# Performance work log

Hardware: AMD Instinct MI355X
Metric: run time of the kernel (lower is better)

The kernel has to match this reference:

```python
import jax, jax.numpy as jnp
from jax import lax
import numpy as np

D_MODEL = 768
D_STATE = 64
D_CONV = 4
EXPAND = 2
HEADDIM = 128
NGROUPS = 1
D_INNER = EXPAND * D_MODEL            # 1536
NHEADS = D_INNER // HEADDIM           # 12
D_IN_PROJ = 2 * D_INNER + 2 * NGROUPS * D_STATE + NHEADS  # 3212
CONV_DIM = D_INNER + 2 * NGROUPS * D_STATE                # 1664
BATCH, SEQLEN = 2, 4096
EPS = 1e-5


def setup_inputs() -> dict:
    key = jax.random.key(0)
    ks = jax.random.split(key, 8)
    u = jax.random.normal(ks[0], (BATCH, SEQLEN, D_MODEL), jnp.float32)
    W_in = jax.random.normal(ks[1], (D_IN_PROJ, D_MODEL), jnp.float32) * 0.02
    conv_w = jax.random.normal(ks[2], (CONV_DIM, D_CONV), jnp.float32) * 0.2
    conv_b = jnp.zeros((CONV_DIM,), jnp.float32)
    # dt_bias init as in BaseMambaBlock: inv-softplus of dt ~ logU(dt_min, dt_max)
    dt = jnp.exp(jax.random.uniform(ks[3], (NHEADS,)) * (np.log(0.1) - np.log(0.001)) + np.log(0.001))
    dt = jnp.clip(dt, 1e-4, None)
    dt_bias = dt + jnp.log(-jnp.expm1(-dt))
    A_log = jnp.log(jnp.abs(jax.random.normal(ks[4], (NHEADS,), jnp.float32)))
    Dp = jnp.ones((NHEADS,), jnp.float32)
    norm_w = jnp.ones((D_INNER,), jnp.float32)
    W_out = jax.random.normal(ks[5], (D_MODEL, D_INNER), jnp.float32) * 0.02
    return dict(u=u, W_in=W_in, conv_w=conv_w, conv_b=conv_b, dt_bias=dt_bias,
                A_log=A_log, Dp=Dp, norm_w=norm_w, W_out=W_out)


def _silu(x):
    return x * jax.nn.sigmoid(x)


def _depthwise_causal_conv(x, w, b):
    # x: [B, L, C], w: [C, W], b: [C]. Causal: left-pad W-1, crop to L.
    Bt, L, C = x.shape
    xp = jnp.pad(x, ((0, 0), (D_CONV - 1, 0), (0, 0)))
    # stack D_CONV shifted views: [B, L, C, W]
    taps = jnp.stack([xp[:, k:k + L, :] for k in range(D_CONV)], axis=-1)
    return jnp.einsum('blcw,cw->blc', taps, w) + b


def reference(u, W_in, conv_w, conv_b, dt_bias, A_log, Dp, norm_w, W_out):
    Bt, L, _ = u.shape
    zxbcdt = jnp.einsum('bld,ed->ble', u, W_in)  # [B, L, 3212]
    z = zxbcdt[..., :D_INNER]                                   # [B,L,1536]
    xBC = zxbcdt[..., D_INNER:D_INNER + CONV_DIM]               # [B,L,1664]
    dt = zxbcdt[..., D_INNER + CONV_DIM:]                       # [B,L,H]
    dt = jax.nn.softplus(dt + dt_bias)                          # [B,L,H]

    xBC = _silu(_depthwise_causal_conv(xBC, conv_w, conv_b))
    x = xBC[..., :D_INNER].reshape(Bt, L, NHEADS, HEADDIM)      # [B,L,H,P]
    Bm = xBC[..., D_INNER:D_INNER + NGROUPS * D_STATE]          # [B,L,N] (ngroups=1)
    Cm = xBC[..., D_INNER + NGROUPS * D_STATE:]                 # [B,L,N]

    A = -jnp.exp(A_log)                                         # [H]
    dA = jnp.exp(dt * A)                                        # [B,L,H]

    # time-major scan over the selective-state-space recurrence
    xs = (jnp.swapaxes(x, 0, 1),   # [L,B,H,P]
          jnp.swapaxes(dt, 0, 1),  # [L,B,H]
          jnp.swapaxes(dA, 0, 1),  # [L,B,H]
          jnp.swapaxes(Bm, 0, 1),  # [L,B,N]
          jnp.swapaxes(Cm, 0, 1))  # [L,B,N]

    def step(state, inp):
        x_t, dt_t, dA_t, B_t, C_t = inp
        # state: [B,H,P,N]
        state = state * dA_t[..., None, None] + (dt_t[..., None] * x_t)[..., None] * B_t[:, None, None, :]
        y_t = jnp.einsum('bhpn,bn->bhp', state, C_t)
        return state, y_t

    state0 = jnp.zeros((Bt, NHEADS, HEADDIM, D_STATE), u.dtype)
    _, y = lax.scan(step, state0, xs)                           # y: [L,B,H,P]
    y = jnp.swapaxes(y, 0, 1) + Dp[None, None, :, None] * x     # skip term D*x
    y = y.reshape(Bt, L, D_INNER)

    # RMSNormGated, norm_before_gate=False: normalize(y * silu(z)) * weight
    g = y * _silu(z)
    g = g * jax.lax.rsqrt(jnp.mean(g * g, axis=-1, keepdims=True) + EPS) * norm_w
    return jnp.einsum('bli,di->bld', g, W_out)
```

## Files before the change

kernel.cpp:

```cpp
#include <hip/hip_runtime.h>
#include <hip/hip_bf16.h>
#include <stdint.h>

#define BATCH   2
#define SEQLEN  4096
#define DMODEL  768
#define DSTATE  64
#define DCONV   4
#define HEADDIM 128
#define NHEADS  12
#define DINNER  1536
#define DINPROJ 3212
#define CONVDIM 1664
#define DXBC    1676
#define NPAD1   3328
#define ROWS    (BATCH*SEQLEN)
#define CHUNK   64
#define NCHUNK  (SEQLEN/CHUNK)
#define CROWS   8

typedef __bf16 bf16x8 __attribute__((ext_vector_type(8)));
typedef float  f32x4  __attribute__((ext_vector_type(4)));

__device__ __forceinline__ f32x4 splat4(float v) { return (f32x4){v, v, v, v}; }

__device__ __forceinline__ void load_lds16(const void* g, void* l) {
    __builtin_amdgcn_global_load_lds(
        (const __attribute__((address_space(1))) unsigned int*)g,
        (__attribute__((address_space(3))) unsigned int*)l, 16, 0, 0);
}

__global__ void cvt_bf16_kernel(const float* __restrict__ src,
                                __hip_bfloat16* __restrict__ dst, int n) {
    int i = (blockIdx.x * blockDim.x + threadIdx.x) * 4;
    if (i + 3 < n) {
        float4 v = *(const float4*)(src + i);
        dst[i + 0] = __float2bfloat16(v.x);
        dst[i + 1] = __float2bfloat16(v.y);
        dst[i + 2] = __float2bfloat16(v.z);
        dst[i + 3] = __float2bfloat16(v.w);
    } else {
        for (; i < n; ++i) dst[i] = __float2bfloat16(src[i]);
    }
}

__global__ void padw1_kernel(const float* __restrict__ src,
                             __hip_bfloat16* __restrict__ dst) {
    int i = blockIdx.x * blockDim.x + threadIdx.x;
    if (i >= NPAD1 * DMODEL) return;
    int r = i / DMODEL;
    float v = (r < DINPROJ) ? src[i] : 0.f;
    dst[i] = __float2bfloat16(v);
}

__global__ __launch_bounds__(256) void gemm_bf16_nt(
    const __hip_bfloat16* __restrict__ A,
    const __hip_bfloat16* __restrict__ Bt,
    float* __restrict__ C,
    int M, int Nreal, int K, int ldc)
{
    __shared__ __align__(16) __hip_bfloat16 As[128 * 32];
    __shared__ __align__(16) __hip_bfloat16 Bs[128 * 32];
    const int tid  = threadIdx.x;
    const int lane = tid & 63;
    const int wave = tid >> 6;
    const int wm   = wave >> 1;
    const int wn   = wave & 1;
    const int tm   = blockIdx.x * 128;
    const int tn   = blockIdx.y * 128;

    f32x4 acc[4][4] = {};

    const int lrow = tid >> 2;
    const int lk8  = (tid & 3) * 8;
    const __hip_bfloat16* gA0 = A  + (size_t)(tm + lrow)      * K + lk8;
    const __hip_bfloat16* gA1 = A  + (size_t)(tm + lrow + 64) * K + lk8;
    const __hip_bfloat16* gB0 = Bt + (size_t)(tn + lrow)      * K + lk8;
    const __hip_bfloat16* gB1 = Bt + (size_t)(tn + lrow + 64) * K + lk8;
    __hip_bfloat16* sA0 = As + tid * 8;
    __hip_bfloat16* sA1 = As + tid * 8 + 2048;
    __hip_bfloat16* sB0 = Bs + tid * 8;
    __hip_bfloat16* sB1 = Bs + tid * 8 + 2048;

    const int fr = lane & 15;
    const int fk = (lane >> 4) * 8;

    for (int kk = 0; kk < K; kk += 32) {
        load_lds16(gA0 + kk, sA0);
        load_lds16(gA1 + kk, sA1);
        load_lds16(gB0 + kk, sB0);
        load_lds16(gB1 + kk, sB1);
        __syncthreads();
        bf16x8 af[4], bfr[4];
#pragma unroll
        for (int i = 0; i < 4; ++i) {
            af[i]  = *(const bf16x8*)(As + (wm * 64 + i * 16 + fr) * 32 + fk);
            bfr[i] = *(const bf16x8*)(Bs + (wn * 64 + i * 16 + fr) * 32 + fk);
        }
#pragma unroll
        for (int mi = 0; mi < 4; ++mi)
#pragma unroll
            for (int ni = 0; ni < 4; ++ni)
                acc[mi][ni] = __builtin_amdgcn_mfma_f32_16x16x32_bf16(
                    af[mi], bfr[ni], acc[mi][ni], 0, 0, 0);
        __syncthreads();
    }

    const int rq = (lane >> 4) * 4;
#pragma unroll
    for (int mi = 0; mi < 4; ++mi) {
#pragma unroll
        for (int ni = 0; ni < 4; ++ni) {
            int col = tn + wn * 64 + ni * 16 + fr;
            if (col < Nreal) {
                size_t rbase = (size_t)(tm + wm * 64 + mi * 16 + rq) * ldc + col;
#pragma unroll
                for (int j = 0; j < 4; ++j)
                    C[rbase + (size_t)j * ldc] = acc[mi][ni][j];
            }
        }
    }
}

__global__ __launch_bounds__(256) void gemm1_fused(
    const __hip_bfloat16* __restrict__ A,
    const __hip_bfloat16* __restrict__ Bt,
    float* __restrict__ Cz,
    float* __restrict__ Cx)
{
    __shared__ __align__(16) __hip_bfloat16 As[128 * 32];
    __shared__ __align__(16) __hip_bfloat16 Bs[128 * 32];
    const int tid  = threadIdx.x;
    const int lane = tid & 63;
    const int wave = tid >> 6;
    const int wm   = wave >> 1;
    const int wn   = wave & 1;
    const int tm   = blockIdx.x * 128;
    const int tn   = blockIdx.y * 128;
    const int K    = DMODEL;

    float* Co;
    int ldc2, cb, nb;
    if (tn < DINNER) { Co = Cz; ldc2 = DINNER; cb = tn;          nb = DINNER; }
    else             { Co = Cx; ldc2 = DXBC;   cb = tn - DINNER; nb = DXBC;   }

    f32x4 acc[4][4] = {};

    const int lrow = tid >> 2;
    const int lk8  = (tid & 3) * 8;
    const __hip_bfloat16* gA0 = A  + (size_t)(tm + lrow)      * K + lk8;
    const __hip_bfloat16* gA1 = A  + (size_t)(tm + lrow + 64) * K + lk8;
    const __hip_bfloat16* gB0 = Bt + (size_t)(tn + lrow)      * K + lk8;
    const __hip_bfloat16* gB1 = Bt + (size_t)(tn + lrow + 64) * K + lk8;
    __hip_bfloat16* sA0 = As + tid * 8;
    __hip_bfloat16* sA1 = As + tid * 8 + 2048;
    __hip_bfloat16* sB0 = Bs + tid * 8;
    __hip_bfloat16* sB1 = Bs + tid * 8 + 2048;

    const int fr = lane & 15;
    const int fk = (lane >> 4) * 8;

    for (int kk = 0; kk < K; kk += 32) {
        load_lds16(gA0 + kk, sA0);
        load_lds16(gA1 + kk, sA1);
        load_lds16(gB0 + kk, sB0);
        load_lds16(gB1 + kk, sB1);
        __syncthreads();
        bf16x8 af[4], bfr[4];
#pragma unroll
        for (int i = 0; i < 4; ++i) {
            af[i]  = *(const bf16x8*)(As + (wm * 64 + i * 16 + fr) * 32 + fk);
            bfr[i] = *(const bf16x8*)(Bs + (wn * 64 + i * 16 + fr) * 32 + fk);
        }
#pragma unroll
        for (int mi = 0; mi < 4; ++mi)
#pragma unroll
            for (int ni = 0; ni < 4; ++ni)
                acc[mi][ni] = __builtin_amdgcn_mfma_f32_16x16x32_bf16(
                    af[mi], bfr[ni], acc[mi][ni], 0, 0, 0);
        __syncthreads();
    }

    const int rq = (lane >> 4) * 4;
#pragma unroll
    for (int mi = 0; mi < 4; ++mi) {
#pragma unroll
        for (int ni = 0; ni < 4; ++ni) {
            int col = cb + wn * 64 + ni * 16 + fr;
            if (col < nb) {
                size_t rbase = (size_t)(tm + wm * 64 + mi * 16 + rq) * ldc2 + col;
#pragma unroll
                for (int j = 0; j < 4; ++j)
                    Co[rbase + (size_t)j * ldc2] = acc[mi][ni][j];
            }
        }
    }
}

__global__ void conv_kernel(const float* __restrict__ xbcdt,
                            const float* __restrict__ convw,
                            const float* __restrict__ convb,
                            float* __restrict__ xbuf,
                            float* __restrict__ Bm,
                            float* __restrict__ Cm)
{
    int c = blockIdx.x * 256 + threadIdx.x;
    if (c >= CONVDIM) return;
    size_t row0 = (size_t)blockIdx.y * CROWS;
    int l0 = (int)(row0 & (SEQLEN - 1));
    float w0 = convw[c * 4 + 0];
    float w1 = convw[c * 4 + 1];
    float w2 = convw[c * 4 + 2];
    float w3 = convw[c * 4 + 3];
    float bias = convb[c];
    const float* src = xbcdt + row0 * DXBC + c;
    float x0 = (l0 >= 3) ? src[-3 * DXBC] : 0.f;
    float x1 = (l0 >= 2) ? src[-2 * DXBC] : 0.f;
    float x2 = (l0 >= 1) ? src[-1 * DXBC] : 0.f;
#pragma unroll
    for (int r = 0; r < CROWS; ++r) {
        float x3 = src[(size_t)r * DXBC];
        float acc = bias + x0 * w0 + x1 * w1 + x2 * w2 + x3 * w3;
        float v = acc / (1.f + __expf(-acc));
        size_t row = row0 + r;
        if (c < DINNER)               xbuf[row * DINNER + c] = v;
        else if (c < DINNER + DSTATE) Bm[row * DSTATE + (c - DINNER)] = v;
        else                          Cm[row * DSTATE + (c - DINNER - DSTATE)] = v;
        x0 = x1; x1 = x2; x2 = x3;
    }
}

__global__ void dt_kernel(const float* __restrict__ xbcdt,
                          const float* __restrict__ dt_bias,
                          const float* __restrict__ A_log,
                          float* __restrict__ dtb, float* __restrict__ dAb)
{
    int i = blockIdx.x * 256 + threadIdx.x;
    if (i >= ROWS * NHEADS) return;
    int row = i / NHEADS, h = i - row * NHEADS;
    float v = xbcdt[(size_t)row * DXBC + CONVDIM + h] + dt_bias[h];
    float dt = (v > 20.f) ? v : log1pf(__expf(v));
    float A = -__expf(A_log[h]);
    dtb[i] = dt;
    dAb[i] = __expf(dt * A);
}

__global__ __launch_bounds__(256) void chunk_state_f32(
    const float* __restrict__ xbuf, const float* __restrict__ Bm,
    const float* __restrict__ dtb, const float* __restrict__ dAb,
    float* __restrict__ Sloc, float* __restrict__ Pk)
{
    const int blk = blockIdx.x;
    const int k   = blk % NCHUNK;
    const int bh  = blk / NCHUNK;
    const int h   = bh % NHEADS;
    const int b   = bh / NHEADS;
    const int tid = threadIdx.x;
    const int pg  = tid >> 3;
    const int n0  = (tid & 7) * 8;
    const size_t row0 = (size_t)b * SEQLEN + k * CHUNK;
    const float* xbase = xbuf + (row0 * NHEADS + h) * HEADDIM + pg * 4;

    __shared__ __align__(16) float lB[CHUNK][DSTATE];
    __shared__ float lDA[CHUNK];
    __shared__ float ldt[CHUNK];

    for (int i = tid; i < CHUNK * DSTATE / 4; i += 256)
        ((float4*)&lB[0][0])[i] = ((const float4*)(Bm + row0 * DSTATE))[i];
    if (tid < CHUNK) {
        lDA[tid] = dAb[(row0 + tid) * NHEADS + h];
        ldt[tid] = dtb[(row0 + tid) * NHEADS + h];
    }
    __syncthreads();

    f32x4 s4[4][2] = {};
    f32x4 xt0[4], xt1[4];

#pragma unroll
    for (int tt = 0; tt < 4; ++tt)
        xt0[tt] = *(const f32x4*)(xbase + (size_t)tt * (NHEADS * HEADDIM));

#pragma unroll
    for (int tile = 0; tile < 16; ++tile) {
        f32x4* cur = (tile & 1) ? xt1 : xt0;
        f32x4* nxt = (tile & 1) ? xt0 : xt1;
        if (tile < 15) {
#pragma unroll
            for (int tt = 0; tt < 4; ++tt)
                nxt[tt] = *(const f32x4*)(xbase +
                    (size_t)((tile + 1) * 4 + tt) * (NHEADS * HEADDIM));
        }
#pragma unroll
        for (int tt = 0; tt < 4; ++tt) {
            int t = tile * 4 + tt;
            f32x4 da4 = splat4(lDA[t]);
            float dtv = ldt[t];
            f32x4 bv0 = *(const f32x4*)&lB[t][n0];
            f32x4 bv1 = *(const f32x4*)&lB[t][n0 + 4];
#pragma unroll
            for (int pl = 0; pl < 4; ++pl) {
                f32x4 dtx = splat4(dtv * cur[tt][pl]);
                s4[pl][0] = s4[pl][0] * da4 + dtx * bv0;
                s4[pl][1] = s4[pl][1] * da4 + dtx * bv1;
            }
        }
    }

    const size_t kbase = (size_t)(bh * NCHUNK + k) * (HEADDIM * DSTATE);
#pragma unroll
    for (int pl = 0; pl < 4; ++pl) {
        size_t a = kbase + (size_t)(pg * 4 + pl) * DSTATE + n0;
        *(f32x4*)(Sloc + a)     = s4[pl][0];
        *(f32x4*)(Sloc + a + 4) = s4[pl][1];
    }

    if (tid == 0) {
        float pr = 1.f;
#pragma unroll 8
        for (int t = 0; t < CHUNK; ++t) pr *= lDA[t];
        Pk[bh * NCHUNK + k] = pr;
    }
}

__global__ __launch_bounds__(256) void scan_phase2(
    float* __restrict__ Sloc, const float* __restrict__ Pk)
{
    int bh = blockIdx.x >> 5;
    int eo = (blockIdx.x & 31) * 256 + threadIdx.x;
    __shared__ float lP[NCHUNK];
    if (threadIdx.x < NCHUNK) lP[threadIdx.x] = Pk[bh * NCHUNK + threadIdx.x];
    __syncthreads();
    float s = 0.f;
    size_t base = (size_t)bh * NCHUNK * 8192 + eo;
#pragma unroll 8
    for (int k = 0; k < NCHUNK; ++k) {
        size_t a = base + (size_t)k * 8192;
        float f = Sloc[a];
        Sloc[a] = s;
        s = s * lP[k] + f;
    }
}

__global__ __launch_bounds__(256) void chunk_y_f32(
    const float* __restrict__ xbuf, const float* __restrict__ Bm,
    const float* __restrict__ Cm, const float* __restrict__ dtb,
    const float* __restrict__ dAb, const float* __restrict__ Dp,
    const float* __restrict__ Sini, float* __restrict__ ybuf)
{
    const int blk = blockIdx.x;
    const int kp  = blk % (NCHUNK / 2);
    const int bh  = blk / (NCHUNK / 2);
    const int h   = bh % NHEADS;
    const int b   = bh / NHEADS;
    const int tid = threadIdx.x;
    const int sub = tid >> 7;
    const int t2  = tid & 127;
    const int pg  = t2 >> 2;
    const int q   = t2 & 3;
    const int n0  = q * 16;
    const int ro  = sub * CHUNK;
    const size_t prow0 = (size_t)b * SEQLEN + (size_t)kp * 2 * CHUNK;
    const size_t row0  = prow0 + ro;
    const float* xbase = xbuf + (row0 * NHEADS + h) * HEADDIM + pg * 4;
    float* ybase = ybuf + (row0 * NHEADS + h) * HEADDIM + pg * 4;

    __shared__ __align__(16) float lB[2 * CHUNK][DSTATE];
    __shared__ __align__(16) float lC[2 * CHUNK][DSTATE];
    __shared__ float lDA[2 * CHUNK];
    __shared__ float ldt[2 * CHUNK];

    for (int i = tid; i < 2 * CHUNK * DSTATE / 4; i += 256) {
        ((float4*)&lB[0][0])[i] = ((const float4*)(Bm + prow0 * DSTATE))[i];
        ((float4*)&lC[0][0])[i] = ((const float4*)(Cm + prow0 * DSTATE))[i];
    }
    if (tid < 2 * CHUNK) {
        lDA[tid] = dAb[(prow0 + tid) * NHEADS + h];
        ldt[tid] = dtb[(prow0 + tid) * NHEADS + h];
    }

    f32x4 s4[4][4];
    const size_t kbase = (size_t)(bh * NCHUNK + kp * 2 + sub) * (HEADDIM * DSTATE);
#pragma unroll
    for (int pl = 0; pl < 4; ++pl) {
        size_t a = kbase + (size_t)(pg * 4 + pl) * DSTATE + n0;
#pragma unroll
        for (int nq = 0; nq < 4; ++nq)
            s4[pl][nq] = *(const f32x4*)(Sini + a + nq * 4);
    }
    const float dph = Dp[h];

    f32x4 xt0[4], xt1[4];
#pragma unroll
    for (int tt = 0; tt < 4; ++tt)
        xt0[tt] = *(const f32x4*)(xbase + (size_t)tt * (NHEADS * HEADDIM));
    __syncthreads();

#pragma unroll
    for (int tile = 0; tile < 16; ++tile) {
        f32x4* cur = (tile & 1) ? xt1 : xt0;
        f32x4* nxt = (tile & 1) ? xt0 : xt1;
        if (tile < 15) {
#pragma unroll
            for (int tt = 0; tt < 4; ++tt)
                nxt[tt] = *(const f32x4*)(xbase +
                    (size_t)((tile + 1) * 4 + tt) * (NHEADS * HEADDIM));
        }
#pragma unroll
        for (int tt = 0; tt < 4; ++tt) {
            int t = tile * 4 + tt;
            int tr = ro + t;
            f32x4 da4 = splat4(lDA[tr]);
            float dtv = ldt[tr];
            f32x4 bv0 = *(const f32x4*)&lB[tr][n0];
            f32x4 bv1 = *(const f32x4*)&lB[tr][n0 + 4];
            f32x4 bv2 = *(const f32x4*)&lB[tr][n0 + 8];
            f32x4 bv3 = *(const f32x4*)&lB[tr][n0 + 12];
            f32x4 cv0 = *(const f32x4*)&lC[tr][n0];
            f32x4 cv1 = *(const f32x4*)&lC[tr][n0 + 4];
            f32x4 cv2 = *(const f32x4*)&lC[tr][n0 + 8];
            f32x4 cv3 = *(const f32x4*)&lC[tr][n0 + 12];
            float yr[4];
#pragma unroll
            for (int pl = 0; pl < 4; ++pl) {
                f32x4 dtx = splat4(dtv * cur[tt][pl]);
                f32x4 v0 = s4[pl][0] * da4 + dtx * bv0;
                f32x4 v1 = s4[pl][1] * da4 + dtx * bv1;
                f32x4 v2 = s4[pl][2] * da4 + dtx * bv2;
                f32x4 v3 = s4[pl][3] * da4 + dtx * bv3;
                s4[pl][0] = v0; s4[pl][1] = v1; s4[pl][2] = v2; s4[pl][3] = v3;
                f32x4 y4 = cv0 * v0 + cv1 * v1 + cv2 * v2 + cv3 * v3;
                float y = (y4[0] + y4[1]) + (y4[2] + y4[3]);
                y += __shfl_xor(y, 1);
                y += __shfl_xor(y, 2);
                yr[pl] = y;
            }
            if (q == 0) {
                f32x4 w = {yr[0] + dph * cur[tt][0], yr[1] + dph * cur[tt][1],
                           yr[2] + dph * cur[tt][2], yr[3] + dph * cur[tt][3]};
                *(f32x4*)(ybase + (size_t)t * (NHEADS * HEADDIM)) = w;
            }
        }
    }
}

#define NT 64
__global__ __launch_bounds__(256) void scan_kernel(
    const float* __restrict__ xbuf, const float* __restrict__ Bm,
    const float* __restrict__ Cm, const float* __restrict__ dtb,
    const float* __restrict__ dAb, const float* __restrict__ Dp,
    float* __restrict__ ybuf)
{
    int blk = blockIdx.x;
    int ps = blk & 7;
    int h  = (blk >> 3) % NHEADS;
    int b  = blk / (NHEADS * 8);
    int p0 = ps * 16;
    int tid = threadIdx.x;
    int pl  = tid >> 4;
    int n0  = (tid & 15) * 4;

    __shared__ __align__(16) float lB[NT][64];
    __shared__ __align__(16) float lC[NT][64];
    __shared__ __align__(16) float lDtx[NT][16];
    __shared__ float lDA[NT];
    __shared__ float lY[NT][16];

    float s0 = 0.f, s1 = 0.f, s2 = 0.f, s3 = 0.f;
    float dph = Dp[h];
    size_t rowbase = (size_t)b * SEQLEN;

    for (int t0 = 0; t0 < SEQLEN; t0 += NT) {
        for (int i = tid; i < NT * 64 / 4; i += 256) {
            ((float4*)&lB[0][0])[i] = ((const float4*)Bm)[(rowbase + t0) * 16 + i];
            ((float4*)&lC[0][0])[i] = ((const float4*)Cm)[(rowbase + t0) * 16 + i];
        }
        for (int i = tid; i < NT * 16; i += 256) {
            int t = i >> 4, pp = i & 15;
            size_t r = rowbase + t0 + t;
            lDtx[t][pp] = dtb[r * NHEADS + h] * xbuf[(r * NHEADS + h) * HEADDIM + p0 + pp];
        }
        if (tid < NT) lDA[tid] = dAb[(rowbase + t0 + tid) * NHEADS + h];
        __syncthreads();

        for (int t = 0; t < NT; ++t) {
            float da  = lDA[t];
            float dtx = lDtx[t][pl];
            const float* bp = &lB[t][n0];
            const float* cp = &lC[t][n0];
            s0 = s0 * da + dtx * bp[0];
            s1 = s1 * da + dtx * bp[1];
            s2 = s2 * da + dtx * bp[2];
            s3 = s3 * da + dtx * bp[3];
            float part = s0 * cp[0] + s1 * cp[1] + s2 * cp[2] + s3 * cp[3];
            part += __shfl_xor(part, 1);
            part += __shfl_xor(part, 2);
            part += __shfl_xor(part, 4);
            part += __shfl_xor(part, 8);
            if ((tid & 15) == 0) lY[t][pl] = part;
        }
        __syncthreads();

        for (int i = tid; i < NT * 16; i += 256) {
            int t = i >> 4, pp = i & 15;
            size_t r = rowbase + t0 + t;
            size_t gi = (r * NHEADS + h) * HEADDIM + p0 + pp;
            ybuf[gi] = lY[t][pp] + dph * xbuf[gi];
        }
        __syncthreads();
    }
}

__global__ __launch_bounds__(256) void gate_rms_kernel(
    const float* __restrict__ ybuf, const float* __restrict__ zbuf,
    const float* __restrict__ norm_w, __hip_bfloat16* __restrict__ gbf)
{
    int row = blockIdx.x;
    int tid = threadIdx.x;
    const float2* y2 = (const float2*)(ybuf + (size_t)row * DINNER);
    const float2* z2 = (const float2*)(zbuf + (size_t)row * DINNER);
    const float2* nw2 = (const float2*)norm_w;
    float g[6];
    float ss = 0.f;
#pragma unroll
    for (int j = 0; j < 3; ++j) {
        int idx = tid + j * 256;
        float2 yy = y2[idx];
        float2 zz = z2[idx];
        float g0 = yy.x * (zz.x / (1.f + __expf(-zz.x)));
        float g1 = yy.y * (zz.y / (1.f + __expf(-zz.y)));
        g[j * 2 + 0] = g0;
        g[j * 2 + 1] = g1;
        ss += g0 * g0 + g1 * g1;
    }
#pragma unroll
    for (int m = 1; m < 64; m <<= 1) ss += __shfl_xor(ss, m);
    __shared__ float red[4];
    if ((tid & 63) == 0) red[tid >> 6] = ss;
    __syncthreads();
    float tot = red[0] + red[1] + red[2] + red[3];
    float scale = rsqrtf(tot * (1.f / DINNER) + 1e-5f);
#pragma unroll
    for (int j = 0; j < 3; ++j) {
        int idx = tid + j * 256;
        float2 w = nw2[idx];
        __hip_bfloat162 o;
        o.x = __float2bfloat16(g[j * 2 + 0] * scale * w.x);
        o.y = __float2bfloat16(g[j * 2 + 1] * scale * w.y);
        *(__hip_bfloat162*)(gbf + (size_t)row * DINNER + idx * 2) = o;
    }
}

extern "C" void kernel_launch(void* const* d_in, const int* in_sizes, int n_in,
                              void* d_out, int out_size, void* d_ws, size_t ws_size,
                              hipStream_t stream)
{
    const float* u       = (const float*)d_in[0];
    const float* W_in    = (const float*)d_in[1];
    const float* conv_w  = (const float*)d_in[2];
    const float* conv_b  = (const float*)d_in[3];
    const float* dt_bias = (const float*)d_in[4];
    const float* A_log   = (const float*)d_in[5];
    const float* Dp      = (const float*)d_in[6];
    const float* norm_w  = (const float*)d_in[7];
    const float* W_out   = (const float*)d_in[8];
    float* out = (float*)d_out;

    char* ws = (char*)d_ws;
    size_t off = 0;
    auto alloc = [&](size_t bytes) {
        char* p = ws + off;
        off += (bytes + 255) & ~(size_t)255;
        return p;
    };
    __hip_bfloat16* ubf  = (__hip_bfloat16*)alloc((size_t)ROWS * DMODEL * 2);
    __hip_bfloat16* W1bf = (__hip_bfloat16*)alloc((size_t)NPAD1 * DMODEL * 2);
    __hip_bfloat16* W2bf = (__hip_bfloat16*)alloc((size_t)DMODEL * DINNER * 2);
    float* zbuf  = (float*)alloc((size_t)ROWS * DINNER * 4);
    float* xbcdt = (float*)alloc((size_t)ROWS * DXBC * 4);
    float* xbuf = (float*)alloc((size_t)ROWS * DINNER * 4);
    float* Bmb  = (float*)alloc((size_t)ROWS * DSTATE * 4);
    float* Cmb  = (float*)alloc((size_t)ROWS * DSTATE * 4);
    float* dtb  = (float*)alloc((size_t)ROWS * NHEADS * 4);
    float* dAb  = (float*)alloc((size_t)ROWS * NHEADS * 4);
    float* ybuf = (float*)alloc((size_t)ROWS * DINNER * 4);
    float* Pkb  = (float*)alloc((size_t)BATCH * NHEADS * NCHUNK * 4);
    __hip_bfloat16* gbf = (__hip_bfloat16*)xbuf;
    float* Sloc = (float*)xbcdt;
    bool chunked = (off <= ws_size);

    cvt_bf16_kernel<<<(ROWS * DMODEL / 4 + 255) / 256, 256, 0, stream>>>(u, ubf, ROWS * DMODEL);
    padw1_kernel<<<(NPAD1 * DMODEL + 255) / 256, 256, 0, stream>>>(W_in, W1bf);
    cvt_bf16_kernel<<<(DMODEL * DINNER / 4 + 255) / 256, 256, 0, stream>>>(W_out, W2bf, DMODEL * DINNER);

    gemm1_fused<<<dim3(ROWS / 128, NPAD1 / 128), 256, 0, stream>>>(
        ubf, W1bf, zbuf, xbcdt);

    conv_kernel<<<dim3((CONVDIM + 255) / 256, ROWS / CROWS), 256, 0, stream>>>(
        xbcdt, conv_w, conv_b, xbuf, Bmb, Cmb);

    dt_kernel<<<(ROWS * NHEADS + 255) / 256, 256, 0, stream>>>(xbcdt, dt_bias, A_log, dtb, dAb);

    if (chunked) {
        chunk_state_f32<<<BATCH * NHEADS * NCHUNK, 256, 0, stream>>>(
            xbuf, Bmb, dtb, dAb, Sloc, Pkb);
        scan_phase2<<<BATCH * NHEADS * 32, 256, 0, stream>>>(Sloc, Pkb);
        chunk_y_f32<<<BATCH * NHEADS * NCHUNK / 2, 256, 0, stream>>>(
            xbuf, Bmb, Cmb, dtb, dAb, Dp, Sloc, ybuf);
    } else {
        scan_kernel<<<BATCH * NHEADS * 8, 256, 0, stream>>>(
            xbuf, Bmb, Cmb, dtb, dAb, Dp, ybuf);
    }

    gate_rms_kernel<<<ROWS, 256, 0, stream>>>(ybuf, zbuf, norm_w, gbf);

    gemm_bf16_nt<<<dim3(ROWS / 128, DMODEL / 128), 256, 0, stream>>>(
        gbf, W2bf, out, ROWS, DMODEL, DINNER, DMODEL);
}
```

Before: 322.2 us.

## Double-buffer LDS tiles and XOR-swizzle K columns in bf16 GEMMs

Both bf16 MFMA GEMM kernels now keep two LDS buffers per operand, so the global-to-LDS load of the next K slice is issued before the current slice's MFMAs run. This removes one barrier per iteration and overlaps memory traffic with compute. The global source column is XOR-swizzled by row and the fragment reads use the matching swizzle, which is meant to spread LDS bank accesses. The cost is twice the LDS per block, which may limit occupancy.

```diff
diff --git a/kernel.cpp b/kernel.cpp
--- a/kernel.cpp
+++ b/kernel.cpp
@@ -18,6 +18,7 @@
 #define CHUNK   64
 #define NCHUNK  (SEQLEN/CHUNK)
 #define CROWS   8
+#define TBUF    4096
 
 typedef __bf16 bf16x8 __attribute__((ext_vector_type(8)));
 typedef float  f32x4  __attribute__((ext_vector_type(4)));
@@ -59,8 +60,8 @@
     float* __restrict__ C,
     int M, int Nreal, int K, int ldc)
 {
-    __shared__ __align__(16) __hip_bfloat16 As[128 * 32];
-    __shared__ __align__(16) __hip_bfloat16 Bs[128 * 32];
+    __shared__ __align__(16) __hip_bfloat16 As[2 * TBUF];
+    __shared__ __align__(16) __hip_bfloat16 Bs[2 * TBUF];
     const int tid  = threadIdx.x;
     const int lane = tid & 63;
     const int wave = tid >> 6;
@@ -72,30 +73,35 @@
     f32x4 acc[4][4] = {};
 
     const int lrow = tid >> 2;
-    const int lk8  = (tid & 3) * 8;
-    const __hip_bfloat16* gA0 = A  + (size_t)(tm + lrow)      * K + lk8;
-    const __hip_bfloat16* gA1 = A  + (size_t)(tm + lrow + 64) * K + lk8;
-    const __hip_bfloat16* gB0 = Bt + (size_t)(tn + lrow)      * K + lk8;
-    const __hip_bfloat16* gB1 = Bt + (size_t)(tn + lrow + 64) * K + lk8;
-    __hip_bfloat16* sA0 = As + tid * 8;
-    __hip_bfloat16* sA1 = As + tid * 8 + 2048;
-    __hip_bfloat16* sB0 = Bs + tid * 8;
-    __hip_bfloat16* sB1 = Bs + tid * 8 + 2048;
-
-    const int fr = lane & 15;
-    const int fk = (lane >> 4) * 8;
-
+    const int lk8s = ((tid & 3) * 8) ^ (((tid >> 3) & 3) << 3);
+    const __hip_bfloat16* gA0 = A  + (size_t)(tm + lrow)      * K + lk8s;
+    const __hip_bfloat16* gA1 = A  + (size_t)(tm + lrow + 64) * K + lk8s;
+    const __hip_bfloat16* gB0 = Bt + (size_t)(tn + lrow)      * K + lk8s;
+    const __hip_bfloat16* gB1 = Bt + (size_t)(tn + lrow + 64) * K + lk8s;
+
+    const int fr  = lane & 15;
+    const int fks = ((lane >> 4) * 8) ^ (((lane >> 1) & 3) << 3);
+
+    load_lds16(gA0, As + tid * 8);
+    load_lds16(gA1, As + tid * 8 + 2048);
+    load_lds16(gB0, Bs + tid * 8);
+    load_lds16(gB1, Bs + tid * 8 + 2048);
+    __syncthreads();
+
+    int bufo = 0;
     for (int kk = 0; kk < K; kk += 32) {
-        load_lds16(gA0 + kk, sA0);
-        load_lds16(gA1 + kk, sA1);
-        load_lds16(gB0 + kk, sB0);
-        load_lds16(gB1 + kk, sB1);
-        __syncthreads();
+        const int nbufo = bufo ^ TBUF;
+        if (kk + 32 < K) {
+            load_lds16(gA0 + kk + 32, As + nbufo + tid * 8);
+            load_lds16(gA1 + kk + 32, As + nbufo + tid * 8 + 2048);
+            load_lds16(gB0 + kk + 32, Bs + nbufo + tid * 8);
+            load_lds16(gB1 + kk + 32, Bs + nbufo + tid * 8 + 2048);
+        }
         bf16x8 af[4], bfr[4];
 #pragma unroll
         for (int i = 0; i < 4; ++i) {
-            af[i]  = *(const bf16x8*)(As + (wm * 64 + i * 16 + fr) * 32 + fk);
-            bfr[i] = *(const bf16x8*)(Bs + (wn * 64 + i * 16 + fr) * 32 + fk);
+            af[i]  = *(const bf16x8*)(As + bufo + (wm * 64 + i * 16 + fr) * 32 + fks);
+            bfr[i] = *(const bf16x8*)(Bs + bufo + (wn * 64 + i * 16 + fr) * 32 + fks);
         }
 #pragma unroll
         for (int mi = 0; mi < 4; ++mi)
@@ -104,6 +110,7 @@
                 acc[mi][ni] = __builtin_amdgcn_mfma_f32_16x16x32_bf16(
                     af[mi], bfr[ni], acc[mi][ni], 0, 0, 0);
         __syncthreads();
+        bufo = nbufo;
     }
 
     const int rq = (lane >> 4) * 4;
@@ -128,8 +135,8 @@
     float* __restrict__ Cz,
     float* __restrict__ Cx)
 {
-    __shared__ __align__(16) __hip_bfloat16 As[128 * 32];
-    __shared__ __align__(16) __hip_bfloat16 Bs[128 * 32];
+    __shared__ __align__(16) __hip_bfloat16 As[2 * TBUF];
+    __shared__ __align__(16) __hip_bfloat16 Bs[2 * TBUF];
     const int tid  = threadIdx.x;
     const int lane = tid & 63;
     const int wave = tid >> 6;
@@ -147,30 +154,35 @@
     f32x4 acc[4][4] = {};
 
     const int lrow = tid >> 2;
-    const int lk8  = (tid & 3) * 8;
-    const __hip_bfloat16* gA0 = A  + (size_t)(tm + lrow)      * K + lk8;
-    const __hip_bfloat16* gA1 = A  + (size_t)(tm + lrow + 64) * K + lk8;
-    const __hip_bfloat16* gB0 = Bt + (size_t)(tn + lrow)      * K + lk8;
-    const __hip_bfloat16* gB1 = Bt + (size_t)(tn + lrow + 64) * K + lk8;
-    __hip_bfloat16* sA0 = As + tid * 8;
-    __hip_bfloat16* sA1 = As + tid * 8 + 2048;
-    __hip_bfloat16* sB0 = Bs + tid * 8;
-    __hip_bfloat16* sB1 = Bs + tid * 8 + 2048;
-
-    const int fr = lane & 15;
-    const int fk = (lane >> 4) * 8;
-
+    const int lk8s = ((tid & 3) * 8) ^ (((tid >> 3) & 3) << 3);
+    const __hip_bfloat16* gA0 = A  + (size_t)(tm + lrow)      * K + lk8s;
+    const __hip_bfloat16* gA1 = A  + (size_t)(tm + lrow + 64) * K + lk8s;
+    const __hip_bfloat16* gB0 = Bt + (size_t)(tn + lrow)      * K + lk8s;
+    const __hip_bfloat16* gB1 = Bt + (size_t)(tn + lrow + 64) * K + lk8s;
+
+    const int fr  = lane & 15;
+    const int fks = ((lane >> 4) * 8) ^ (((lane >> 1) & 3) << 3);
+
+    load_lds16(gA0, As + tid * 8);
+    load_lds16(gA1, As + tid * 8 + 2048);
+    load_lds16(gB0, Bs + tid * 8);
+    load_lds16(gB1, Bs + tid * 8 + 2048);
+    __syncthreads();
+
+    int bufo = 0;
     for (int kk = 0; kk < K; kk += 32) {
-        load_lds16(gA0 + kk, sA0);
-        load_lds16(gA1 + kk, sA1);
-        load_lds16(gB0 + kk, sB0);
-        load_lds16(gB1 + kk, sB1);
-        __syncthreads();
+        const int nbufo = bufo ^ TBUF;
+        if (kk + 32 < K) {
+            load_lds16(gA0 + kk + 32, As + nbufo + tid * 8);
+            load_lds16(gA1 + kk + 32, As + nbufo + tid * 8 + 2048);
+            load_lds16(gB0 + kk + 32, Bs + nbufo + tid * 8);
+            load_lds16(gB1 + kk + 32, Bs + nbufo + tid * 8 + 2048);
+        }
         bf16x8 af[4], bfr[4];
 #pragma unroll
         for (int i = 0; i < 4; ++i) {
-            af[i]  = *(const bf16x8*)(As + (wm * 64 + i * 16 + fr) * 32 + fk);
-            bfr[i] = *(const bf16x8*)(Bs + (wn * 64 + i * 16 + fr) * 32 + fk);
+            af[i]  = *(const bf16x8*)(As + bufo + (wm * 64 + i * 16 + fr) * 32 + fks);
+            bfr[i] = *(const bf16x8*)(Bs + bufo + (wn * 64 + i * 16 + fr) * 32 + fks);
         }
 #pragma unroll
         for (int mi = 0; mi < 4; ++mi)
@@ -179,6 +191,7 @@
                 acc[mi][ni] = __builtin_amdgcn_mfma_f32_16x16x32_bf16(
                     af[mi], bfr[ni], acc[mi][ni], 0, 0, 0);
         __syncthreads();
+        bufo = nbufo;
     }
 
     const int rq = (lane >> 4) * 4;
```

Result: faster. 302.2 us (-6.2%).
